# Optimization experiments

Hardware: AMD Instinct MI355X
Metric: run time of the kernel (lower is better)

Reference implementation:

```python
import jax, jax.numpy as jnp
import numpy as np

N_CAT = 100000
N_USERS = 50000
N_REL = 32
D = 64
E = 1600000
NNZ = 1000000


def setup_inputs() -> dict:
    key = jax.random.key(0)
    ks = jax.random.split(key, 8)
    category_emb = jax.random.normal(ks[0], (N_CAT, D), dtype=jnp.float32)
    user_emb = jax.random.normal(ks[1], (N_USERS, D), dtype=jnp.float32)
    edge_index = jax.random.randint(ks[2], (2, E), 0, N_CAT, dtype=jnp.int64)
    edge_type = jax.random.randint(ks[3], (E,), 1, N_REL + 1, dtype=jnp.int64)  # 1-indexed relations
    im_rows = jax.random.randint(ks[4], (NNZ,), 0, N_USERS, dtype=jnp.int64)
    im_cols = jax.random.randint(ks[5], (NNZ,), 0, N_CAT, dtype=jnp.int64)
    im_vals = jax.random.uniform(ks[6], (NNZ,), dtype=jnp.float32)
    weight = jax.random.normal(ks[7], (N_REL, D), dtype=jnp.float32)
    return {"category_emb": category_emb, "user_emb": user_emb,
            "edge_index": edge_index, "edge_type": edge_type,
            "im_rows": im_rows, "im_cols": im_cols, "im_vals": im_vals,
            "weight": weight}


def reference(category_emb, user_emb, edge_index, edge_type, im_rows, im_cols, im_vals, weight):
    n_categories = category_emb.shape[0]
    n_users = user_emb.shape[0]
    head, tail = edge_index[0], edge_index[1]

    edge_relation_emb = weight[edge_type - 1]                      # [E, D]
    neigh_relation_emb = category_emb[tail] * edge_relation_emb    # [E, D]

    # attention weight: (||h*r|| * ||t*r||)^2 per edge -> scalar per edge
    hr = jnp.linalg.norm(category_emb[head] * edge_relation_emb, axis=1)  # [E]
    tr = jnp.linalg.norm(neigh_relation_emb, axis=1)                      # [E]
    att = (hr * tr) ** 2                                                  # [E]

    # scatter_softmax over edges grouped by head node
    grp_max = jax.ops.segment_max(att, head, num_segments=n_categories)   # [N_CAT]
    e = jnp.exp(att - grp_max[head])                                      # [E]
    grp_sum = jax.ops.segment_sum(e, head, num_segments=n_categories)     # [N_CAT]
    w = e / grp_sum[head]                                                 # [E]

    # scatter_sum aggregation to heads
    category_agg = jax.ops.segment_sum(w[:, None] * neigh_relation_emb,
                                       head, num_segments=n_categories)   # [N_CAT, D]

    # sparse interact_mat @ category_emb (COO)
    user_agg = jax.ops.segment_sum(im_vals[:, None] * category_emb[im_cols],
                                   im_rows, num_segments=n_users)         # [N_USERS, D]

    score = jax.nn.softmax(user_emb @ weight.T, axis=-1)                   # [N_USERS, N_REL]
    user_agg = user_agg + (score @ weight) * user_agg
    return (category_agg, user_agg)
```

## Files before the change

### kernel.cpp

```cpp
#include <hip/hip_runtime.h>
#include <hip/hip_bf16.h>
#include <hip/hip_fp16.h>
#include <float.h>
#include <stdint.h>

#define N_CAT   100000
#define N_USERS 50000
#define N_REL   32
#define D       64
#define NEDGE   1600000
#define NNZ     1000000

#define EB_SHIFT 9
#define EB_SIZE  512
#define NBKE     ((N_CAT + EB_SIZE - 1) / EB_SIZE)
#define UB_SHIFT 8
#define UB_SIZE  256
#define NBKU     ((N_USERS + UB_SIZE - 1) / UB_SIZE)
#define NBK      (NBKE + NBKU)

#define T1   4096
#define ECAP 15360
#define UCAP 7680


__device__ __forceinline__ unsigned int pack_half2(float a, float b) {
    return (unsigned int)__half_as_ushort(__float2half_rn(a)) |
           ((unsigned int)__half_as_ushort(__float2half_rn(b)) << 16);
}

template<int F16>
__device__ __forceinline__ float cat_val(const float* __restrict__ cat,
                                         const __half* __restrict__ cath,
                                         size_t idx) {
    return F16 ? __half2float(cath[idx]) : cat[idx];
}

template<int W16>
__global__ __launch_bounds__(256) void norm2_kernel(
        const float* __restrict__ cat,
        const float* __restrict__ W,
        float* __restrict__ norm2,
        unsigned short* __restrict__ cath) {
    __shared__ float4 w2[N_REL * 16];
    int t = threadIdx.x;
    const float4* Wv = (const float4*)W;
    for (int i = t; i < N_REL * 16; i += 256) {
        float4 v = Wv[i];
        v.x *= v.x; v.y *= v.y; v.z *= v.z; v.w *= v.w;
        w2[i] = v;
    }
    __syncthreads();

    int node = blockIdx.x * 64 + (t >> 2);
    int q    = t & 3;
    if (node >= N_CAT) return;

    const float4* catv = (const float4*)cat;
    float acc[N_REL];
#pragma unroll
    for (int r = 0; r < N_REL; ++r) acc[r] = 0.f;

    uint2 hp[4];
#pragma unroll
    for (int c = 0; c < 4; ++c) {
        float4 xv = catv[(size_t)node * 16 + q * 4 + c];
        if (W16) {
            hp[c].x = pack_half2(xv.x, xv.y);
            hp[c].y = pack_half2(xv.z, xv.w);
        }
        xv.x *= xv.x; xv.y *= xv.y; xv.z *= xv.z; xv.w *= xv.w;
#pragma unroll
        for (int r = 0; r < N_REL; ++r) {
            float4 wv = w2[r * 16 + q * 4 + c];
            acc[r] += xv.x * wv.x + xv.y * wv.y + xv.z * wv.z + xv.w * wv.w;
        }
    }
    if (W16) {
        uint4* cv16 = (uint4*)cath;
        cv16[(size_t)node * 8 + q * 2]     = make_uint4(hp[0].x, hp[0].y, hp[1].x, hp[1].y);
        cv16[(size_t)node * 8 + q * 2 + 1] = make_uint4(hp[2].x, hp[2].y, hp[3].x, hp[3].y);
    }
#pragma unroll
    for (int r = 0; r < N_REL; ++r) {
        acc[r] += __shfl_xor(acc[r], 1);
        acc[r] += __shfl_xor(acc[r], 2);
    }
    float4* nv = (float4*)norm2;
    size_t base = (size_t)node * 8 + q * 2;
    if (q == 0) {
        nv[base]     = make_float4(acc[0],  acc[1],  acc[2],  acc[3]);
        nv[base + 1] = make_float4(acc[4],  acc[5],  acc[6],  acc[7]);
    } else if (q == 1) {
        nv[base]     = make_float4(acc[8],  acc[9],  acc[10], acc[11]);
        nv[base + 1] = make_float4(acc[12], acc[13], acc[14], acc[15]);
    } else if (q == 2) {
        nv[base]     = make_float4(acc[16], acc[17], acc[18], acc[19]);
        nv[base + 1] = make_float4(acc[20], acc[21], acc[22], acc[23]);
    } else {
        nv[base]     = make_float4(acc[24], acc[25], acc[26], acc[27]);
        nv[base + 1] = make_float4(acc[28], acc[29], acc[30], acc[31]);
    }
}

__global__ void coarse_hist_kernel(const int* __restrict__ head,
                                   const int* __restrict__ imr,
                                   int* __restrict__ ccnt) {
    __shared__ int h[NBK];
    int t = threadIdx.x;
    for (int i = t; i < NBK; i += 256) h[i] = 0;
    __syncthreads();
    int stride = gridDim.x * 256;
    for (int i = blockIdx.x * 256 + t; i < NEDGE + NNZ; i += stride) {
        if (i < NEDGE) atomicAdd(&h[head[i] >> EB_SHIFT], 1);
        else           atomicAdd(&h[NBKE + (imr[i - NEDGE] >> UB_SHIFT)], 1);
    }
    __syncthreads();
    for (int i = t; i < NBK; i += 256) if (h[i]) atomicAdd(&ccnt[i], h[i]);
}

__global__ void coarse_scan_kernel(const int* __restrict__ ccnt,
                                   int* __restrict__ cbase_e, int* __restrict__ cbase_u,
                                   int* __restrict__ ccur_e,  int* __restrict__ ccur_u,
                                   int* __restrict__ offs_e,  int* __restrict__ offs_u) {
    __shared__ int sc[256];
    int t = threadIdx.x;
    int c = (t < NBKE) ? ccnt[t] : 0;
    sc[t] = c; __syncthreads();
    for (int off = 1; off < 256; off <<= 1) {
        int v = (t >= off) ? sc[t - off] : 0; __syncthreads();
        sc[t] += v; __syncthreads();
    }
    int excl = sc[t] - c;
    if (t < NBKE) { cbase_e[t] = excl; ccur_e[t] = excl; }
    if (t == NBKE - 1) cbase_e[NBKE] = excl + c;
    __syncthreads();
    c = (t < NBKU) ? ccnt[NBKE + t] : 0;
    sc[t] = c; __syncthreads();
    for (int off = 1; off < 256; off <<= 1) {
        int v = (t >= off) ? sc[t - off] : 0; __syncthreads();
        sc[t] += v; __syncthreads();
    }
    excl = sc[t] - c;
    if (t < NBKU) { cbase_u[t] = excl; ccur_u[t] = excl; }
    if (t == NBKU - 1) cbase_u[NBKU] = excl + c;
    if (t == 0) { offs_e[N_CAT] = NEDGE; offs_u[N_USERS] = NNZ; }
}

__global__ __launch_bounds__(256) void pass1_edges_kernel(
        const int* __restrict__ head, const int* __restrict__ tail,
        const int* __restrict__ etype, int* __restrict__ ccur_e,
        int* __restrict__ sorted_ta) {
    __shared__ int cnt[256], loc[256], base[256], sc[256];
    __shared__ int stage[T1];
    __shared__ int gpos[T1];
    int t = threadIdx.x;
    int tile = blockIdx.x * T1;
    cnt[t] = 0;
    __syncthreads();
    int rec[16], bk[16];
#pragma unroll
    for (int k = 0; k < 16; ++k) {
        int i = tile + k * 256 + t;
        if (i < NEDGE) {
            int h = head[i], tl = tail[i], r = etype[i] - 1;
            bk[k]  = h >> EB_SHIFT;
            rec[k] = ((h & (EB_SIZE - 1)) << 22) | (tl << 5) | r;
            atomicAdd(&cnt[bk[k]], 1);
        } else bk[k] = -1;
    }
    __syncthreads();
    int c = cnt[t];
    sc[t] = c; __syncthreads();
    for (int off = 1; off < 256; off <<= 1) {
        int v = (t >= off) ? sc[t - off] : 0; __syncthreads();
        sc[t] += v; __syncthreads();
    }
    loc[t] = sc[t] - c;
    if (t < NBKE && c > 0) base[t] = atomicAdd(&ccur_e[t], c);
    __syncthreads();
    cnt[t] = loc[t];
    __syncthreads();
#pragma unroll
    for (int k = 0; k < 16; ++k) {
        if (bk[k] >= 0) {
            int p = atomicAdd(&cnt[bk[k]], 1);
            stage[p] = rec[k];
            gpos[p]  = base[bk[k]] + (p - loc[bk[k]]);
        }
    }
    __syncthreads();
    int nv = min(T1, NEDGE - tile);
    for (int i = t; i < nv; i += 256) sorted_ta[gpos[i]] = stage[i];
}

__global__ __launch_bounds__(256) void pass1_users_kernel(
        const int* __restrict__ imr, const int* __restrict__ imc,
        const float* __restrict__ imv, int* __restrict__ ccur_u,
        int2* __restrict__ sorted_cv) {
    __shared__ int cnt[256], loc[256], base[256], sc[256];
    __shared__ int2 stage[T1];
    __shared__ int gpos[T1];
    int t = threadIdx.x;
    int tile = blockIdx.x * T1;
    cnt[t] = 0;
    __syncthreads();
    int2 rec[16]; int bk[16];
#pragma unroll
    for (int k = 0; k < 16; ++k) {
        int i = tile + k * 256 + t;
        if (i < NNZ) {
            int rr = imr[i];
            bk[k]  = rr >> UB_SHIFT;
            rec[k] = make_int2(((rr & (UB_SIZE - 1)) << 17) | imc[i],
                               __float_as_int(imv[i]));
            atomicAdd(&cnt[bk[k]], 1);
        } else bk[k] = -1;
    }
    __syncthreads();
    int c = cnt[t];
    sc[t] = c; __syncthreads();
    for (int off = 1; off < 256; off <<= 1) {
        int v = (t >= off) ? sc[t - off] : 0; __syncthreads();
        sc[t] += v; __syncthreads();
    }
    loc[t] = sc[t] - c;
    if (t < NBKU && c > 0) base[t] = atomicAdd(&ccur_u[t], c);
    __syncthreads();
    cnt[t] = loc[t];
    __syncthreads();
#pragma unroll
    for (int k = 0; k < 16; ++k) {
        if (bk[k] >= 0) {
            int p = atomicAdd(&cnt[bk[k]], 1);
            stage[p] = rec[k];
            gpos[p]  = base[bk[k]] + (p - loc[bk[k]]);
        }
    }
    __syncthreads();
    int nv = min(T1, NNZ - tile);
    for (int i = t; i < nv; i += 256) sorted_cv[gpos[i]] = stage[i];
}

__global__ __launch_bounds__(256) void pass2_kernel(
        const int* __restrict__ cbase_e, const int* __restrict__ cbase_u,
        int* __restrict__ offs_e, int* __restrict__ offs_u,
        int* __restrict__ sorted_ta, int2* __restrict__ sorted_cv) {
    __shared__ int lds[UCAP * 2];
    __shared__ int fh[EB_SIZE + 1];
    __shared__ int sc[256];
    int t = threadIdx.x;
    int b = blockIdx.x;
    if (b < NBKE) {
        int h0 = b << EB_SHIFT;
        int start = cbase_e[b], end = cbase_e[b + 1];
        int n = min(end - start, ECAP);
        for (int i = t; i < n; i += 256) lds[i] = sorted_ta[start + i];
        fh[2 * t] = 0; fh[2 * t + 1] = 0;
        __syncthreads();
        for (int i = t; i < n; i += 256) atomicAdd(&fh[lds[i] >> 22], 1);
        __syncthreads();
        int a = fh[2 * t], b2 = fh[2 * t + 1];
        sc[t] = a + b2; __syncthreads();
        for (int off = 1; off < 256; off <<= 1) {
            int v = (t >= off) ? sc[t - off] : 0; __syncthreads();
            sc[t] += v; __syncthreads();
        }
        int pe = sc[t] - (a + b2);
        int lim = min(EB_SIZE, N_CAT - h0);
        if (2 * t     < lim) offs_e[h0 + 2 * t]     = start + pe;
        if (2 * t + 1 < lim) offs_e[h0 + 2 * t + 1] = start + pe + a;
        fh[2 * t] = pe; fh[2 * t + 1] = pe + a;
        __syncthreads();
        for (int i = t; i < n; i += 256) {
            int rec = lds[i];
            int p = atomicAdd(&fh[rec >> 22], 1);
            sorted_ta[start + p] = rec & 0x3FFFFF;
        }
    } else {
        int k = b - NBKE;
        int u0 = k << UB_SHIFT;
        int start = cbase_u[k], end = cbase_u[k + 1];
        int n = min(end - start, UCAP);
        int2* lds2 = (int2*)lds;
        for (int i = t; i < n; i += 256) lds2[i] = sorted_cv[start + i];
        fh[t] = 0;
        __syncthreads();
        for (int i = t; i < n; i += 256) atomicAdd(&fh[lds2[i].x >> 17], 1);
        __syncthreads();
        int c = fh[t];
        sc[t] = c; __syncthreads();
        for (int off = 1; off < 256; off <<= 1) {
            int v = (t >= off) ? sc[t - off] : 0; __syncthreads();
            sc[t] += v; __syncthreads();
        }
        int excl = sc[t] - c;
        int lim = min(UB_SIZE, N_USERS - u0);
        if (t < lim) offs_u[u0 + t] = start + excl;
        fh[t] = excl;
        __syncthreads();
        for (int i = t; i < n; i += 256) {
            int2 rec = lds2[i];
            int p = atomicAdd(&fh[rec.x >> 17], 1);
            sorted_cv[start + p] = make_int2(rec.x & 0x1FFFF, rec.y);
        }
    }
}

template<int F16>
__global__ void cat_agg_sorted_kernel(const int* __restrict__ offs_e,
                                      const int* __restrict__ sorted_ta,
                                      const float* __restrict__ norm2,
                                      const float* __restrict__ cat,
                                      const __half* __restrict__ cath,
                                      const float* __restrict__ W,
                                      float* __restrict__ cat_agg) {
    __shared__ float sW[N_REL * D];
    for (int i = threadIdx.x; i < N_REL * D; i += 256) sW[i] = W[i];
    __syncthreads();

    int wv   = threadIdx.x >> 6;
    int lane = threadIdx.x & 63;
    int h = blockIdx.x * 4 + wv;
    int start = offs_e[h];
    int end   = offs_e[h + 1];
    int deg   = end - start;

    float a0 = 0.f, a1 = 0.f, a2 = 0.f, a3 = 0.f;

    if (deg <= 64) {
        int   rec = 0;
        float att = -FLT_MAX;
        if (lane < deg) {
            rec = sorted_ta[start + lane];
            int tt = rec >> 5, r = rec & 31;
            att = norm2[h * N_REL + r] * norm2[(size_t)tt * N_REL + r];
        }
        float m = att;
#pragma unroll
        for (int off = 32; off > 0; off >>= 1) m = fmaxf(m, __shfl_xor(m, off));
        float ex = (lane < deg) ? __expf(att - m) : 0.f;
        float ssum = ex;
#pragma unroll
        for (int off = 32; off > 0; off >>= 1) ssum += __shfl_xor(ssum, off);
        float w = (deg > 0) ? ex / ssum : 0.f;

        int j = 0;
        for (; j + 4 <= deg; j += 4) {
            int   tr0 = __shfl(rec, j + 0), tr1 = __shfl(rec, j + 1);
            int   tr2 = __shfl(rec, j + 2), tr3 = __shfl(rec, j + 3);
            float w0  = __shfl(w,   j + 0), w1  = __shfl(w,   j + 1);
            float w2  = __shfl(w,   j + 2), w3  = __shfl(w,   j + 3);
            a0 += w0 * cat_val<F16>(cat, cath, (size_t)(tr0 >> 5) * D + lane) * sW[(tr0 & 31) * D + lane];
            a1 += w1 * cat_val<F16>(cat, cath, (size_t)(tr1 >> 5) * D + lane) * sW[(tr1 & 31) * D + lane];
            a2 += w2 * cat_val<F16>(cat, cath, (size_t)(tr2 >> 5) * D + lane) * sW[(tr2 & 31) * D + lane];
            a3 += w3 * cat_val<F16>(cat, cath, (size_t)(tr3 >> 5) * D + lane) * sW[(tr3 & 31) * D + lane];
        }
        for (; j < deg; ++j) {
            int   tr = __shfl(rec, j);
            float ww = __shfl(w,   j);
            a0 += ww * cat_val<F16>(cat, cath, (size_t)(tr >> 5) * D + lane) * sW[(tr & 31) * D + lane];
        }
    } else {
        float m = -FLT_MAX;
        for (int j = lane; j < deg; j += 64) {
            int rec = sorted_ta[start + j];
            int tt = rec >> 5, r = rec & 31;
            m = fmaxf(m, norm2[h * N_REL + r] * norm2[(size_t)tt * N_REL + r]);
        }
#pragma unroll
        for (int off = 32; off > 0; off >>= 1) m = fmaxf(m, __shfl_xor(m, off));
        float ssum = 0.f;
        for (int j = lane; j < deg; j += 64) {
            int rec = sorted_ta[start + j];
            int tt = rec >> 5, r = rec & 31;
            ssum += __expf(norm2[h * N_REL + r] * norm2[(size_t)tt * N_REL + r] - m);
        }
#pragma unroll
        for (int off = 32; off > 0; off >>= 1) ssum += __shfl_xor(ssum, off);
        float inv = 1.f / ssum;
        for (int j0 = 0; j0 < deg; j0 += 64) {
            int n = min(64, deg - j0);
            int   rec = 0;
            float w   = 0.f;
            if (lane < n) {
                rec = sorted_ta[start + j0 + lane];
                int tt = rec >> 5, r = rec & 31;
                w = __expf(norm2[h * N_REL + r] * norm2[(size_t)tt * N_REL + r] - m) * inv;
            }
            for (int j = 0; j < n; ++j) {
                int   tr = __shfl(rec, j);
                float ww = __shfl(w,   j);
                a0 += ww * cat_val<F16>(cat, cath, (size_t)(tr >> 5) * D + lane) * sW[(tr & 31) * D + lane];
            }
        }
    }
    cat_agg[(size_t)h * D + lane] = (a0 + a1) + (a2 + a3);
}

template<int F16>
__global__ void spmm_user_kernel(const int* __restrict__ offs_u,
                                 const int2* __restrict__ sorted_cv,
                                 const float* __restrict__ cat,
                                 const __half* __restrict__ cath,
                                 const float* __restrict__ uemb,
                                 const float* __restrict__ W,
                                 float* __restrict__ uagg) {
    __shared__ float s_user[4][D];
    __shared__ float s_score[4][N_REL];
    int wv   = threadIdx.x >> 6;
    int lane = threadIdx.x & 63;
    int u = blockIdx.x * 4 + wv;
    int start = offs_u[u];
    int end   = offs_u[u + 1];
    int deg   = end - start;

    float a0 = 0.f, a1 = 0.f, a2 = 0.f, a3 = 0.f;
    for (int j0 = 0; j0 < deg; j0 += 64) {
        int n = min(64, deg - j0);
        int   my_c = 0;
        float my_v = 0.f;
        if (lane < n) {
            int2 cv = sorted_cv[start + j0 + lane];
            my_c = cv.x;
            my_v = __int_as_float(cv.y);
        }
        int j = 0;
        for (; j + 4 <= n; j += 4) {
            int   c0 = __shfl(my_c, j + 0), c1 = __shfl(my_c, j + 1);
            int   c2 = __shfl(my_c, j + 2), c3 = __shfl(my_c, j + 3);
            float v0 = __shfl(my_v, j + 0), v1 = __shfl(my_v, j + 1);
            float v2 = __shfl(my_v, j + 2), v3 = __shfl(my_v, j + 3);
            a0 += v0 * cat_val<F16>(cat, cath, (size_t)c0 * D + lane);
            a1 += v1 * cat_val<F16>(cat, cath, (size_t)c1 * D + lane);
            a2 += v2 * cat_val<F16>(cat, cath, (size_t)c2 * D + lane);
            a3 += v3 * cat_val<F16>(cat, cath, (size_t)c3 * D + lane);
        }
        for (; j < n; ++j) {
            int   cc = __shfl(my_c, j);
            float vv = __shfl(my_v, j);
            a0 += vv * cat_val<F16>(cat, cath, (size_t)cc * D + lane);
        }
    }
    float acc = (a0 + a1) + (a2 + a3);

    s_user[wv][lane] = uemb[(size_t)u * D + lane];
    __syncthreads();

    if (lane < N_REL) {
        float dot = 0.f;
#pragma unroll
        for (int d = 0; d < D; ++d) dot += s_user[wv][d] * W[lane * D + d];
        float mm = dot;
#pragma unroll
        for (int off = 16; off > 0; off >>= 1) mm = fmaxf(mm, __shfl_xor(mm, off));
        float ex = __expf(dot - mm);
        float sm = ex;
#pragma unroll
        for (int off = 16; off > 0; off >>= 1) sm += __shfl_xor(sm, off);
        s_score[wv][lane] = ex / sm;
    }
    __syncthreads();

    float proj = 0.f;
#pragma unroll
    for (int r = 0; r < N_REL; ++r) proj += s_score[wv][r] * W[r * D + lane];

    uagg[(size_t)u * D + lane] = acc * (1.f + proj);
}

extern "C" void kernel_launch(void* const* d_in, const int* in_sizes, int n_in,
                              void* d_out, int out_size, void* d_ws, size_t ws_size,
                              hipStream_t stream) {
    const float* cat   = (const float*)d_in[0];
    const float* uemb  = (const float*)d_in[1];
    const int*   eidx  = (const int*)d_in[2];
    const int*   etype = (const int*)d_in[3];
    const int*   imr   = (const int*)d_in[4];
    const int*   imc   = (const int*)d_in[5];
    const float* imv   = (const float*)d_in[6];
    const float* W     = (const float*)d_in[7];
    const int* head = eidx;
    const int* tail = eidx + NEDGE;

    float* out     = (float*)d_out;
    float* cat_agg = out;
    float* uagg    = out + (size_t)N_CAT * D;

    float* norm2   = (float*)d_ws;
    int*   ccnt    = (int*)(norm2 + (size_t)N_CAT * N_REL);
    int*   cbase_e = ccnt + NBK;
    int*   cbase_u = cbase_e + NBKE + 1;
    int*   ccur_e  = cbase_u + NBKU + 1;
    int*   ccur_u  = ccur_e + NBKE;
    int*   offs_e  = ccur_u + NBKU;
    int*   offs_u  = offs_e + N_CAT + 1;
    int*   sorted_ta = offs_u + N_USERS + 1;
    int2*  sorted_cv = (int2*)(sorted_ta + NEDGE);

    unsigned short* cath_us =
        (unsigned short*)(((uintptr_t)(sorted_cv + NNZ) + 255) & ~(uintptr_t)255);
    size_t need = (size_t)((char*)(cath_us + (size_t)N_CAT * D) - (char*)d_ws);
    int use16 = (ws_size >= need);

    hipMemsetAsync(ccnt, 0, (size_t)NBK * sizeof(int), stream);

    coarse_hist_kernel<<<512, 256, 0, stream>>>(head, imr, ccnt);
    coarse_scan_kernel<<<1, 256, 0, stream>>>(ccnt, cbase_e, cbase_u,
                                              ccur_e, ccur_u, offs_e, offs_u);
    pass1_edges_kernel<<<(NEDGE + T1 - 1) / T1, 256, 0, stream>>>(
        head, tail, etype, ccur_e, sorted_ta);
    pass1_users_kernel<<<(NNZ + T1 - 1) / T1, 256, 0, stream>>>(
        imr, imc, imv, ccur_u, sorted_cv);
    pass2_kernel<<<NBK, 256, 0, stream>>>(cbase_e, cbase_u, offs_e, offs_u,
                                          sorted_ta, sorted_cv);
    if (use16) {
        norm2_kernel<1><<<(N_CAT + 63) / 64, 256, 0, stream>>>(cat, W, norm2, cath_us);
        cat_agg_sorted_kernel<1><<<N_CAT / 4, 256, 0, stream>>>(
            offs_e, sorted_ta, norm2, cat, (const __half*)cath_us, W, cat_agg);
        spmm_user_kernel<1><<<N_USERS / 4, 256, 0, stream>>>(
            offs_u, sorted_cv, cat, (const __half*)cath_us, uemb, W, uagg);
    } else {
        norm2_kernel<0><<<(N_CAT + 63) / 64, 256, 0, stream>>>(cat, W, norm2, nullptr);
        cat_agg_sorted_kernel<0><<<N_CAT / 4, 256, 0, stream>>>(
            offs_e, sorted_ta, norm2, cat, nullptr, W, cat_agg);
        spmm_user_kernel<0><<<N_USERS / 4, 256, 0, stream>>>(
            offs_u, sorted_cv, cat, nullptr, uemb, W, uagg);
    }
}
```

Measured before the change: 373.9 us.

## Process 8 neighbor rows per wavefront with 16-byte vector loads in gather kernels

Both gather kernels, the category aggregation and the user SpMM, now split each 64-lane wavefront into 8 groups of 8 lanes. Each group loads a whole 64-dim row with one 16-byte load per lane (8 halves or 8 floats), and two rows are processed per iteration, so 16 neighbors are in flight at once instead of 4 scalar per-lane loads. Partial sums are combined across groups with xor shuffles, and the output is written as float4 from the first group. The relation weights are staged in padded shared memory (stride 17 float4) to reduce bank conflicts. This adds a cross-group reduction and leaves lanes idle in the final partial chunk of low-degree rows.

```diff
diff --git a/kernel.cpp b/kernel.cpp
--- a/kernel.cpp
+++ b/kernel.cpp
@@ -23,6 +23,8 @@
 #define ECAP 15360
 #define UCAP 7680
 
+#define WSTRIDE 17
+
 
 __device__ __forceinline__ unsigned int pack_half2(float a, float b) {
     return (unsigned int)__half_as_ushort(__float2half_rn(a)) |
@@ -30,10 +32,24 @@
 }
 
 template<int F16>
-__device__ __forceinline__ float cat_val(const float* __restrict__ cat,
-                                         const __half* __restrict__ cath,
-                                         size_t idx) {
-    return F16 ? __half2float(cath[idx]) : cat[idx];
+__device__ __forceinline__ void load_row8(const float4* __restrict__ catv4,
+                                          const uint4* __restrict__ cath4,
+                                          int row, int gl, float f[8]) {
+    if (F16) {
+        uint4 h = cath4[(size_t)row * 8 + gl];
+        const __half2* hp = (const __half2*)&h;
+        float2 a = __half22float2(hp[0]);
+        float2 b = __half22float2(hp[1]);
+        float2 c = __half22float2(hp[2]);
+        float2 d = __half22float2(hp[3]);
+        f[0] = a.x; f[1] = a.y; f[2] = b.x; f[3] = b.y;
+        f[4] = c.x; f[5] = c.y; f[6] = d.x; f[7] = d.y;
+    } else {
+        float4 a = catv4[(size_t)row * 16 + gl * 2];
+        float4 b = catv4[(size_t)row * 16 + gl * 2 + 1];
+        f[0] = a.x; f[1] = a.y; f[2] = a.z; f[3] = a.w;
+        f[4] = b.x; f[5] = b.y; f[6] = b.z; f[7] = b.w;
+    }
 }
 
 template<int W16>
@@ -308,25 +324,35 @@
 }
 
 template<int F16>
-__global__ void cat_agg_sorted_kernel(const int* __restrict__ offs_e,
-                                      const int* __restrict__ sorted_ta,
-                                      const float* __restrict__ norm2,
-                                      const float* __restrict__ cat,
-                                      const __half* __restrict__ cath,
-                                      const float* __restrict__ W,
-                                      float* __restrict__ cat_agg) {
-    __shared__ float sW[N_REL * D];
-    for (int i = threadIdx.x; i < N_REL * D; i += 256) sW[i] = W[i];
-    __syncthreads();
-
+__global__ __launch_bounds__(256) void cat_agg_sorted_kernel(
+        const int* __restrict__ offs_e,
+        const int* __restrict__ sorted_ta,
+        const float* __restrict__ norm2,
+        const float* __restrict__ cat,
+        const uint4* __restrict__ cath4,
+        const float* __restrict__ W,
+        float* __restrict__ cat_agg) {
+    __shared__ float4 sW4[N_REL * WSTRIDE];
+    {
+        const float4* Wv = (const float4*)W;
+        for (int i = threadIdx.x; i < N_REL * 16; i += 256)
+            sW4[(i >> 4) * WSTRIDE + (i & 15)] = Wv[i];
+    }
+    __syncthreads();
+
+    const float4* catv4 = (const float4*)cat;
     int wv   = threadIdx.x >> 6;
     int lane = threadIdx.x & 63;
+    int grp  = lane >> 3;
+    int gl   = lane & 7;
     int h = blockIdx.x * 4 + wv;
     int start = offs_e[h];
     int end   = offs_e[h + 1];
     int deg   = end - start;
 
-    float a0 = 0.f, a1 = 0.f, a2 = 0.f, a3 = 0.f;
+    float accA[8], accB[8];
+#pragma unroll
+    for (int k = 0; k < 8; ++k) { accA[k] = 0.f; accB[k] = 0.f; }
 
     if (deg <= 64) {
         int   rec = 0;
@@ -345,21 +371,26 @@
         for (int off = 32; off > 0; off >>= 1) ssum += __shfl_xor(ssum, off);
         float w = (deg > 0) ? ex / ssum : 0.f;
 
-        int j = 0;
-        for (; j + 4 <= deg; j += 4) {
-            int   tr0 = __shfl(rec, j + 0), tr1 = __shfl(rec, j + 1);
-            int   tr2 = __shfl(rec, j + 2), tr3 = __shfl(rec, j + 3);
-            float w0  = __shfl(w,   j + 0), w1  = __shfl(w,   j + 1);
-            float w2  = __shfl(w,   j + 2), w3  = __shfl(w,   j + 3);
-            a0 += w0 * cat_val<F16>(cat, cath, (size_t)(tr0 >> 5) * D + lane) * sW[(tr0 & 31) * D + lane];
-            a1 += w1 * cat_val<F16>(cat, cath, (size_t)(tr1 >> 5) * D + lane) * sW[(tr1 & 31) * D + lane];
-            a2 += w2 * cat_val<F16>(cat, cath, (size_t)(tr2 >> 5) * D + lane) * sW[(tr2 & 31) * D + lane];
-            a3 += w3 * cat_val<F16>(cat, cath, (size_t)(tr3 >> 5) * D + lane) * sW[(tr3 & 31) * D + lane];
-        }
-        for (; j < deg; ++j) {
-            int   tr = __shfl(rec, j);
-            float ww = __shfl(w,   j);
-            a0 += ww * cat_val<F16>(cat, cath, (size_t)(tr >> 5) * D + lane) * sW[(tr & 31) * D + lane];
+        for (int e = 0; e < deg; e += 16) {
+            int   tA = __shfl(rec, e + grp);
+            float wA = __shfl(w,   e + grp);
+            int   tB = __shfl(rec, e + 8 + grp);
+            float wB = __shfl(w,   e + 8 + grp);
+            float fA[8], fB[8];
+            load_row8<F16>(catv4, cath4, tA >> 5, gl, fA);
+            load_row8<F16>(catv4, cath4, tB >> 5, gl, fB);
+            const float4* wrA = &sW4[(tA & 31) * WSTRIDE + gl * 2];
+            const float4* wrB = &sW4[(tB & 31) * WSTRIDE + gl * 2];
+            float4 wa0 = wrA[0], wa1 = wrA[1];
+            float4 wb0 = wrB[0], wb1 = wrB[1];
+            accA[0] += wA * fA[0] * wa0.x;  accA[1] += wA * fA[1] * wa0.y;
+            accA[2] += wA * fA[2] * wa0.z;  accA[3] += wA * fA[3] * wa0.w;
+            accA[4] += wA * fA[4] * wa1.x;  accA[5] += wA * fA[5] * wa1.y;
+            accA[6] += wA * fA[6] * wa1.z;  accA[7] += wA * fA[7] * wa1.w;
+            accB[0] += wB * fB[0] * wb0.x;  accB[1] += wB * fB[1] * wb0.y;
+            accB[2] += wB * fB[2] * wb0.z;  accB[3] += wB * fB[3] * wb0.w;
+            accB[4] += wB * fB[4] * wb1.x;  accB[5] += wB * fB[5] * wb1.y;
+            accB[6] += wB * fB[6] * wb1.z;  accB[7] += wB * fB[7] * wb1.w;
         }
     } else {
         float m = -FLT_MAX;
@@ -388,34 +419,79 @@
                 int tt = rec >> 5, r = rec & 31;
                 w = __expf(norm2[h * N_REL + r] * norm2[(size_t)tt * N_REL + r] - m) * inv;
             }
-            for (int j = 0; j < n; ++j) {
-                int   tr = __shfl(rec, j);
-                float ww = __shfl(w,   j);
-                a0 += ww * cat_val<F16>(cat, cath, (size_t)(tr >> 5) * D + lane) * sW[(tr & 31) * D + lane];
+            for (int e = 0; e < n; e += 16) {
+                int   tA = __shfl(rec, e + grp);
+                float wA = __shfl(w,   e + grp);
+                int   tB = __shfl(rec, e + 8 + grp);
+                float wB = __shfl(w,   e + 8 + grp);
+                float fA[8], fB[8];
+                load_row8<F16>(catv4, cath4, tA >> 5, gl, fA);
+                load_row8<F16>(catv4, cath4, tB >> 5, gl, fB);
+                const float4* wrA = &sW4[(tA & 31) * WSTRIDE + gl * 2];
+                const float4* wrB = &sW4[(tB & 31) * WSTRIDE + gl * 2];
+                float4 wa0 = wrA[0], wa1 = wrA[1];
+                float4 wb0 = wrB[0], wb1 = wrB[1];
+                accA[0] += wA * fA[0] * wa0.x;  accA[1] += wA * fA[1] * wa0.y;
+                accA[2] += wA * fA[2] * wa0.z;  accA[3] += wA * fA[3] * wa0.w;
+                accA[4] += wA * fA[4] * wa1.x;  accA[5] += wA * fA[5] * wa1.y;
+                accA[6] += wA * fA[6] * wa1.z;  accA[7] += wA * fA[7] * wa1.w;
+                accB[0] += wB * fB[0] * wb0.x;  accB[1] += wB * fB[1] * wb0.y;
+                accB[2] += wB * fB[2] * wb0.z;  accB[3] += wB * fB[3] * wb0.w;
+                accB[4] += wB * fB[4] * wb1.x;  accB[5] += wB * fB[5] * wb1.y;
+                accB[6] += wB * fB[6] * wb1.z;  accB[7] += wB * fB[7] * wb1.w;
             }
         }
     }
-    cat_agg[(size_t)h * D + lane] = (a0 + a1) + (a2 + a3);
+
+    float o[8];
+#pragma unroll
+    for (int k = 0; k < 8; ++k) {
+        float v = accA[k] + accB[k];
+        v += __shfl_xor(v, 8);
+        v += __shfl_xor(v, 16);
+        v += __shfl_xor(v, 32);
+        o[k] = v;
+    }
+    if (grp == 0) {
+        float4* outv = (float4*)&cat_agg[(size_t)h * D];
+        outv[gl * 2]     = make_float4(o[0], o[1], o[2], o[3]);
+        outv[gl * 2 + 1] = make_float4(o[4], o[5], o[6], o[7]);
+    }
 }
 
 template<int F16>
-__global__ void spmm_user_kernel(const int* __restrict__ offs_u,
-                                 const int2* __restrict__ sorted_cv,
-                                 const float* __restrict__ cat,
-                                 const __half* __restrict__ cath,
-                                 const float* __restrict__ uemb,
-                                 const float* __restrict__ W,
-                                 float* __restrict__ uagg) {
-    __shared__ float s_user[4][D];
-    __shared__ float s_score[4][N_REL];
+__global__ __launch_bounds__(256) void spmm_user_kernel(
+        const int* __restrict__ offs_u,
+        const int2* __restrict__ sorted_cv,
+        const float* __restrict__ cat,
+        const uint4* __restrict__ cath4,
+        const float* __restrict__ uemb,
+        const float* __restrict__ W,
+        float* __restrict__ uagg) {
+    __shared__ float4 sW4[N_REL * WSTRIDE];
+    __shared__ float4 s_user4[4][16];
+    __shared__ float  s_score[4][N_REL];
+    {
+        const float4* Wv = (const float4*)W;
+        for (int i = threadIdx.x; i < N_REL * 16; i += 256)
+            sW4[(i >> 4) * WSTRIDE + (i & 15)] = Wv[i];
+    }
+    __syncthreads();
+
+    const float4* catv4 = (const float4*)cat;
     int wv   = threadIdx.x >> 6;
     int lane = threadIdx.x & 63;
+    int grp  = lane >> 3;
+    int gl   = lane & 7;
     int u = blockIdx.x * 4 + wv;
     int start = offs_u[u];
     int end   = offs_u[u + 1];
     int deg   = end - start;
 
-    float a0 = 0.f, a1 = 0.f, a2 = 0.f, a3 = 0.f;
+    float accA[8], accB[8];
+#pragma unroll
+    for (int k = 0; k < 8; ++k) { accA[k] = 0.f; accB[k] = 0.f; }
+
     for (int j0 = 0; j0 < deg; j0 += 64) {
         int n = min(64, deg - j0);
         int   my_c = 0;
@@ -425,32 +501,43 @@
             my_c = cv.x;
             my_v = __int_as_float(cv.y);
         }
-        int j = 0;
-        for (; j + 4 <= n; j += 4) {
-            int   c0 = __shfl(my_c, j + 0), c1 = __shfl(my_c, j + 1);
-            int   c2 = __shfl(my_c, j + 2), c3 = __shfl(my_c, j + 3);
-            float v0 = __shfl(my_v, j + 0), v1 = __shfl(my_v, j + 1);
-            float v2 = __shfl(my_v, j + 2), v3 = __shfl(my_v, j + 3);
-            a0 += v0 * cat_val<F16>(cat, cath, (size_t)c0 * D + lane);
-            a1 += v1 * cat_val<F16>(cat, cath, (size_t)c1 * D + lane);
-            a2 += v2 * cat_val<F16>(cat, cath, (size_t)c2 * D + lane);
-            a3 += v3 * cat_val<F16>(cat, cath, (size_t)c3 * D + lane);
-        }
-        for (; j < n; ++j) {
-            int   cc = __shfl(my_c, j);
-            float vv = __shfl(my_v, j);
-            a0 += vv * cat_val<F16>(cat, cath, (size_t)cc * D + lane);
-        }
-    }
-    float acc = (a0 + a1) + (a2 + a3);
-
-    s_user[wv][lane] = uemb[(size_t)u * D + lane];
+        for (int e = 0; e < n; e += 16) {
+            int   cA = __shfl(my_c, e + grp);
+            float vA = __shfl(my_v, e + grp);
+            int   cB = __shfl(my_c, e + 8 + grp);
+            float vB = __shfl(my_v, e + 8 + grp);
+            float fA[8], fB[8];
+            load_row8<F16>(catv4, cath4, cA, gl, fA);
+            load_row8<F16>(catv4, cath4, cB, gl, fB);
+#pragma unroll
+            for (int k = 0; k < 8; ++k) {
+                accA[k] += vA * fA[k];
+                accB[k] += vB * fB[k];
+            }
+        }
+    }
+
+    float acc[8];
+#pragma unroll
+    for (int k = 0; k < 8; ++k) {
+        float v = accA[k] + accB[k];
+        v += __shfl_xor(v, 8);
+        v += __shfl_xor(v, 16);
+        v += __shfl_xor(v, 32);
+        acc[k] = v;
+    }
+
+    ((float*)s_user4[wv])[lane] = uemb[(size_t)u * D + lane];
     __syncthreads();
 
     if (lane < N_REL) {
         float dot = 0.f;
-#pragma unroll
-        for (int d = 0; d < D; ++d) dot += s_user[wv][d] * W[lane * D + d];
+        const float4* wr = &sW4[lane * WSTRIDE];
+#pragma unroll
+        for (int i = 0; i < 16; ++i) {
+            float4 a = wr[i], b = s_user4[wv][i];
+            dot += a.x * b.x + a.y * b.y + a.z * b.z + a.w * b.w;
+        }
         float mm = dot;
 #pragma unroll
         for (int off = 16; off > 0; off >>= 1) mm = fmaxf(mm, __shfl_xor(mm, off));
@@ -462,11 +549,25 @@
     }
     __syncthreads();
 
-    float proj = 0.f;
-#pragma unroll
-    for (int r = 0; r < N_REL; ++r) proj += s_score[wv][r] * W[r * D + lane];
-
-    uagg[(size_t)u * D + lane] = acc * (1.f + proj);
+    float p[8];
+#pragma unroll
+    for (int k = 0; k < 8; ++k) p[k] = 0.f;
+#pragma unroll
+    for (int r = 0; r < N_REL; ++r) {
+        float s = s_score[wv][r];
+        float4 w0 = sW4[r * WSTRIDE + gl * 2];
+        float4 w1 = sW4[r * WSTRIDE + gl * 2 + 1];
+        p[0] += s * w0.x; p[1] += s * w0.y; p[2] += s * w0.z; p[3] += s * w0.w;
+        p[4] += s * w1.x; p[5] += s * w1.y; p[6] += s * w1.z; p[7] += s * w1.w;
+    }
+
+    if (grp == 0) {
+        float4* ov = (float4*)&uagg[(size_t)u * D];
+        ov[gl * 2]     = make_float4(acc[0] * (1.f + p[0]), acc[1] * (1.f + p[1]),
+                                     acc[2] * (1.f + p[2]), acc[3] * (1.f + p[3]));
+        ov[gl * 2 + 1] = make_float4(acc[4] * (1.f + p[4]), acc[5] * (1.f + p[5]),
+                                     acc[6] * (1.f + p[6]), acc[7] * (1.f + p[7]));
+    }
 }
 
 extern "C" void kernel_launch(void* const* d_in, const int* in_sizes, int n_in,
@@ -517,9 +618,9 @@
     if (use16) {
         norm2_kernel<1><<<(N_CAT + 63) / 64, 256, 0, stream>>>(cat, W, norm2, cath_us);
         cat_agg_sorted_kernel<1><<<N_CAT / 4, 256, 0, stream>>>(
-            offs_e, sorted_ta, norm2, cat, (const __half*)cath_us, W, cat_agg);
+            offs_e, sorted_ta, norm2, cat, (const uint4*)cath_us, W, cat_agg);
         spmm_user_kernel<1><<<N_USERS / 4, 256, 0, stream>>>(
-            offs_u, sorted_cv, cat, (const __half*)cath_us, uemb, W, uagg);
+            offs_u, sorted_cv, cat, (const uint4*)cath_us, uemb, W, uagg);
     } else {
         norm2_kernel<0><<<(N_CAT + 63) / 64, 256, 0, stream>>>(cat, W, norm2, nullptr);
         cat_agg_sorted_kernel<0><<<N_CAT / 4, 256, 0, stream>>>(
```

Result: faster. 339.7 us (-9.2%).
